# Performance work log

Hardware: AMD Instinct MI355X
Metric: run time of the kernel (lower is better)

## Reference

```python
import jax, jax.numpy as jnp
import numpy as np
import math

B, N, D = 128, 64, 2
H, M, L = 64, 64, 2
OMEGA = 1.0


def setup_inputs() -> dict:
    key = jax.random.key(0)
    ks = jax.random.split(key, 32)
    s = 0.1  # param scale
    rn = lambda k, shp: jax.random.normal(k, shp, dtype=jnp.float32) * s
    inp = {
        "x": jax.random.normal(ks[0], (B, N, D), dtype=jnp.float32),
        "spin": jnp.zeros((B, N, 1), jnp.float32),
        "node_w1": rn(ks[1], (D + 1, H)), "node_b1": rn(ks[2], (H,)),
        "node_w2": rn(ks[3], (H, H)), "node_b2": rn(ks[4], (H,)),
        "edge_w1": rn(ks[5], (D + 2, M)), "edge_b1": rn(ks[6], (M,)),
        "edge_w2": rn(ks[7], (M, M)), "edge_b2": rn(ks[8], (M,)),
        "v2e_w1": rn(ks[9], (L, H + M, M)), "v2e_b1": rn(ks[10], (L, M)),
        "v2e_w2": rn(ks[11], (L, M, M)), "v2e_b2": rn(ks[12], (L, M)),
        "e2v_w1": rn(ks[13], (L, M, H)), "e2v_b1": rn(ks[14], (L, H)),
        "e2v_w2": rn(ks[15], (L, H, H)), "e2v_b2": rn(ks[16], (L, H)),
        "head_w1": rn(ks[17], (H, H)), "head_b1": rn(ks[18], (H,)),
        "head_w2": rn(ks[19], (H, D)), "head_b2": rn(ks[20], (D,)),
        # bf_scale_init=0.3 -> softplus-inverse
        "scale": jnp.array([math.log(math.exp(0.3) - 1.0)], jnp.float32),
    }
    return inp


def _mlp(x, w1, b1, w2, b2, act):
    return act(x @ w1 + b1) @ w2 + b2


def reference(x, spin, node_w1, node_b1, node_w2, node_b2,
              edge_w1, edge_b1, edge_w2, edge_b2,
              v2e_w1, v2e_b1, v2e_w2, v2e_b2,
              e2v_w1, e2v_b1, e2v_w2, e2v_b2,
              head_w1, head_b1, head_w2, head_b2, scale):
    gelu = lambda t: jax.nn.gelu(t, approximate=False)  # torch exact GELU
    b, n, d = x.shape
    xs = x * jnp.float32(math.sqrt(OMEGA))
    # node embedding: [B,N,H]
    hv = _mlp(jnp.concatenate([xs, spin], -1), node_w1, node_b1, node_w2, node_b2, gelu)
    # dense pairwise edge features; dr[b,i,j] = xs[b,j] - xs[b,i]
    dr = xs[:, None, :, :] - xs[:, :, None, :]            # [B,N,N,D]
    r2 = jnp.sum(dr * dr, axis=-1, keepdims=True)          # [B,N,N,1]
    rr = jnp.sqrt(r2 + 1e-12)
    he = _mlp(jnp.concatenate([dr, rr, r2], -1), edge_w1, edge_b1, edge_w2, edge_b2, gelu)  # [B,N,N,M]
    # mask excludes self-edges (i==j) from aggregation (they were never created
    # in the original edge list; their dense entries never influence off-diag values)
    mask = (1.0 - jnp.eye(n, dtype=x.dtype))[None, :, :, None]
    inv = jnp.float32(1.0 / max(n - 1, 1))
    for l in range(v2e_w1.shape[0]):
        hvb = jnp.broadcast_to(hv[:, :, None, :], (b, n, n, hv.shape[-1]))  # source node i
        he = _mlp(jnp.concatenate([hvb, he], -1), v2e_w1[l], v2e_b1[l], v2e_w2[l], v2e_b2[l], gelu)
        m = _mlp(he, e2v_w1[l], e2v_b1[l], e2v_w2[l], e2v_b2[l], gelu)      # [B,N,N,H]
        hv = hv + jnp.sum(m * mask, axis=1) * inv           # scatter-add over sources i into j
    dx = _mlp(hv, head_w1, head_b1, head_w2, head_b2, jnp.tanh) * jax.nn.softplus(scale[0])
    return dx - jnp.mean(dx, axis=1, keepdims=True)
```

## Files before the change

kernel.cpp:

```cpp
#include <hip/hip_runtime.h>
#include <math.h>


typedef unsigned short u16;
typedef unsigned int u32;
typedef _Float16 half8 __attribute__((ext_vector_type(8)));
typedef __attribute__((ext_vector_type(4))) float floatx4;

#define TS 72
#define HROW 72
#define HBLK (64 * HROW)

__device__ __forceinline__ float gelu_f(float x) {
    float s = fabsf(x) * 0.70710678118654752f;
    float q = fmaf(fmaf(fmaf(fmaf(0.078108f, s, 0.000972f), s, 0.230389f), s, 0.278393f), s, 1.0f);
    float q2 = q * q;
    float r = __builtin_amdgcn_rcpf(q2 * q2);
    float t = 0.5f * x * r;
    return x > 0.f ? x - t : t;
}

__global__ __launch_bounds__(256) void k_pre(
    const float* __restrict__ ew2, const float* __restrict__ w1he0,
    const float* __restrict__ w2_0, const float* __restrict__ u1_0,
    const float* __restrict__ w1he1, const float* __restrict__ w2_1,
    const float* __restrict__ u1_1,
    const float* __restrict__ eb2, const float* __restrict__ b2_0,
    const float* __restrict__ c1_0, const float* __restrict__ b2_1,
    const float* __restrict__ c1_1,
    const float* __restrict__ b1_0v, const float* __restrict__ b1nv,
    const float* __restrict__ u2_0, const float* __restrict__ u2_1,
    const float* __restrict__ w1n, const float* __restrict__ hw1,
    _Float16* __restrict__ WF,
    float* __restrict__ biasB, float* __restrict__ biasC, float* __restrict__ biasD,
    float* __restrict__ u2_0T, float* __restrict__ u2_1T,
    float* __restrict__ w1nT, float* __restrict__ hw1T,
    const float* __restrict__ x, const float* __restrict__ spin,
    const float* __restrict__ nw1, const float* __restrict__ nb1,
    const float* __restrict__ nw2, const float* __restrict__ nb2,
    const float* __restrict__ w1_0,
    float* __restrict__ hv, float* __restrict__ p0)
{
    int blk = blockIdx.x;
    if (blk < 64) {
        int s = blk >> 4;
        int idx = (blk & 15) * 256 + threadIdx.x;
        int k = idx >> 6, n = idx & 63;
        const float *A, *Bm;
        if (s == 0)      { A = ew2;  Bm = w1he0; }
        else if (s == 1) { A = w2_0; Bm = u1_0;  }
        else if (s == 2) { A = w2_0; Bm = w1he1; }
        else             { A = w2_1; Bm = u1_1;  }
        float acc = 0.f;
        for (int q = 0; q < 64; ++q) acc = fmaf(A[k * 64 + q], Bm[q * 64 + n], acc);
        int kc = k >> 5, qd = (k >> 3) & 3, jj = k & 7;
        WF[(((s * 2 + kc) * 64 + n) * 4 + qd) * 8 + jj] = (_Float16)acc;
    } else if (blk == 64) {
        int s = threadIdx.x >> 6, cc = threadIdx.x & 63;
        if (s > 0) {
            const float *bv, *Bm, *add; float* dst;
            if (s == 1)      { bv = b2_0; Bm = u1_0;  add = c1_0; dst = biasB; }
            else if (s == 2) { bv = b2_0; Bm = w1he1; add = b1nv; dst = biasC; }
            else             { bv = b2_1; Bm = u1_1;  add = c1_1; dst = biasD; }
            float acc = add[cc];
            for (int q = 0; q < 64; ++q) acc = fmaf(bv[q], Bm[q * 64 + cc], acc);
            dst[cc] = acc;
        }
    } else if (blk < 129) {
        int idx = (blk - 65) * 256 + threadIdx.x;
        int s = idx >> 12, r = idx & 4095, m = r >> 6, tc = r & 63;
        const float* W = s == 0 ? u2_0 : s == 1 ? u2_1 : s == 2 ? w1n : hw1;
        float* WT      = s == 0 ? u2_0T : s == 1 ? u2_1T : s == 2 ? w1nT : hw1T;
        WT[tc * 64 + m] = W[m * 64 + tc];
    } else {
        __shared__ float a[4][64];
        __shared__ float shv[4][64];
        int w = threadIdx.x >> 6, h = threadIdx.x & 63;
        int node = (blk - 129) * 4 + w;
        float2 xv = ((const float2*)x)[node];
        float sp = spin[node];
        float z = fmaf(xv.x, nw1[h], fmaf(xv.y, nw1[64 + h], fmaf(sp, nw1[128 + h], nb1[h])));
        a[w][h] = gelu_f(z);
        float acc = nb2[h];
        for (int k = 0; k < 64; ++k) acc = fmaf(a[w][k], nw2[k * 64 + h], acc);
        hv[node * 64 + h] = acc;
        shv[w][h] = acc;
        float pa = b1_0v[h];
        for (int q = 0; q < 64; ++q) pa = fmaf(eb2[q], w1he0[q * 64 + h], pa);
        for (int k = 0; k < 64; ++k) pa = fmaf(shv[w][k], w1_0[k * 64 + h], pa);
        p0[node * 64 + h] = pa;
    }
}

__device__ __forceinline__ void mfma_acc(
    const _Float16* __restrict__ tA, const _Float16* __restrict__ WF,
    int stage, int c, int quad, int nn, floatx4 acc[4])
{
    int sA = ((nn >> 2) & 3) << 3;
    #pragma unroll
    for (int kc = 0; kc < 2; ++kc) {
        half8 bf = *(const half8*)(WF + (((stage * 2 + kc) * 64 + c) * 4 + quad) * 8);
        int k0 = (kc * 32 + quad * 8) ^ sA;
        #pragma unroll
        for (int mt = 0; mt < 4; ++mt) {
            half8 af = *(const half8*)(tA + (mt * 16 + nn) * TS + k0);
            acc[mt] = __builtin_amdgcn_mfma_f32_16x16x32_f16(af, bf, acc[mt], 0, 0, 0);
        }
    }
}

__device__ __forceinline__ void init_bias(floatx4 acc[4], float bc) {
    #pragma unroll
    for (int mt = 0; mt < 4; ++mt) acc[mt] = (floatx4){bc, bc, bc, bc};
}
__device__ __forceinline__ void init_p(floatx4 acc[4], const float* __restrict__ p,
                                       int rowbase, int c, int quad) {
    #pragma unroll
    for (int mt = 0; mt < 4; ++mt)
        #pragma unroll
        for (int r = 0; r < 4; ++r)
            acc[mt][r] = p[(rowbase + mt * 16 + quad * 4 + r) * 64 + c];
}

__global__ __launch_bounds__(256, 8) void k_L0(
    const float* __restrict__ x,
    const float* __restrict__ ew1, const float* __restrict__ eb1,
    const float* __restrict__ p0,
    const float* __restrict__ biasB,
    const float* __restrict__ u2_0T, const float* __restrict__ c2_0,
    const _Float16* __restrict__ WF,
    const float* __restrict__ hv0, float* __restrict__ hv1,
    const float* __restrict__ w1nT, const float* __restrict__ biasC,
    float* __restrict__ p1,
    u16* __restrict__ he0g)
{
    __shared__ __align__(16) _Float16 tA[64 * TS];
    __shared__ float sS[64];
    __shared__ float shv[64];
    __shared__ float sred[256];
    int t = threadIdx.x, L = t & 63;
    int w = __builtin_amdgcn_readfirstlane(t >> 6);
    int nn = L & 15, quad = L >> 4;
    int c = w * 16 + nn;
    int cw = c ^ (quad << 3);
    int b = blockIdx.x >> 6, j = blockIdx.x & 63;

    float2 xi = ((const float2*)x)[b * 64 + L];
    float2 xj = ((const float2*)x)[b * 64 + j];
    float d0 = xj.x - xi.x, d1 = xj.y - xi.y;
    float r2 = fmaf(d0, d0, d1 * d1);
    float rr = sqrtf(r2 + 1e-12f);
    int swL = ((L >> 2) & 3) << 3;

    #pragma unroll
    for (int mb = 0; mb < 2; ++mb) {
        int m0 = w * 16 + mb * 8;
        half8 h8;
        #pragma unroll
        for (int kk = 0; kk < 8; ++kk) {
            int m = m0 + kk;
            float z = fmaf(d0, ew1[m], fmaf(d1, ew1[64 + m],
                      fmaf(rr, ew1[128 + m], fmaf(r2, ew1[192 + m], eb1[m]))));
            h8[kk] = (_Float16)gelu_f(z);
        }
        *(half8*)(tA + L * TS + (m0 ^ swL)) = h8;
    }
    __syncthreads();

    floatx4 acc[4];
    init_p(acc, p0, b * 64, c, quad);
    mfma_acc(tA, WF, 0, c, quad, nn, acc);
    __syncthreads();
    {
        u16* dst = he0g + (size_t)blockIdx.x * HBLK;
        #pragma unroll
        for (int mt = 0; mt < 4; ++mt)
            #pragma unroll
            for (int r = 0; r < 4; ++r) {
                int i = mt * 16 + quad * 4 + r;
                _Float16 y = (_Float16)gelu_f(acc[mt][r]);
                tA[i * TS + cw] = y;
                dst[i * HROW + cw] = __builtin_bit_cast(u16, y);
            }
    }
    __syncthreads();
    init_bias(acc, biasB[c]);
    mfma_acc(tA, WF, 1, c, quad, nn, acc);
    {
        float s = 0.f;
        #pragma unroll
        for (int mt = 0; mt < 4; ++mt)
            #pragma unroll
            for (int r = 0; r < 4; ++r) {
                int i = mt * 16 + quad * 4 + r;
                float g = gelu_f(acc[mt][r]);
                s += (i == j) ? 0.f : g;
            }
        s += __shfl_xor(s, 16);
        s += __shfl_xor(s, 32);
        if (quad == 0) sS[c] = s;
    }
    __syncthreads();
    {
        const float4* sv4 = (const float4*)(sS + w * 16);
        const float4* uv4 = (const float4*)(u2_0T + L * 64 + w * 16);
        float g = 0.f;
        #pragma unroll
        for (int m4 = 0; m4 < 4; ++m4) {
            float4 sv = sv4[m4], uv = uv4[m4];
            g = fmaf(sv.x, uv.x, fmaf(sv.y, uv.y, fmaf(sv.z, uv.z, fmaf(sv.w, uv.w, g))));
        }
        sred[w * 64 + L] = g;
    }
    __syncthreads();
    if (t < 64) {
        float g = sred[t] + sred[64 + t] + sred[128 + t] + sred[192 + t];
        int o = blockIdx.x * 64 + t;
        float hvv = hv0[o] + g * (1.0f / 63.0f) + c2_0[t];
        hv1[o] = hvv;
        shv[t] = hvv;
    }
    __syncthreads();
    {
        const float4* hv4 = (const float4*)(shv + w * 16);
        const float4* wv4 = (const float4*)(w1nT + L * 64 + w * 16);
        float pa = 0.f;
        #pragma unroll
        for (int m4 = 0; m4 < 4; ++m4) {
            float4 sv = hv4[m4], uv = wv4[m4];
            pa = fmaf(sv.x, uv.x, fmaf(sv.y, uv.y, fmaf(sv.z, uv.z, fmaf(sv.w, uv.w, pa))));
        }
        sred[w * 64 + L] = pa;
    }
    __syncthreads();
    if (t < 64)
        p1[blockIdx.x * 64 + t] = biasC[t] + sred[t] + sred[64 + t] + sred[128 + t] + sred[192 + t];
}

__global__ __launch_bounds__(256, 8) void k_L1(
    const u16* __restrict__ he0g,
    const float* __restrict__ p1,
    const float* __restrict__ biasD,
    const float* __restrict__ u2_1T, const float* __restrict__ c2_1,
    const _Float16* __restrict__ WF,
    const float* __restrict__ hv1,
    const float* __restrict__ hw1T, const float* __restrict__ hb1,
    const float* __restrict__ hw2, const float* __restrict__ hb2,
    const float* __restrict__ scale, float* __restrict__ dx)
{
    __shared__ __align__(16) _Float16 tA[64 * TS];
    __shared__ float sS[64];
    __shared__ float shv[64];
    __shared__ float sred[256];
    int t = threadIdx.x, L = t & 63;
    int w = __builtin_amdgcn_readfirstlane(t >> 6);
    int nn = L & 15, quad = L >> 4;
    int c = w * 16 + nn;
    int cw = c ^ (quad << 3);
    int b = blockIdx.x >> 6, j = blockIdx.x & 63;

    {
        const float4* src = (const float4*)(he0g + (size_t)blockIdx.x * HBLK);
        float4* dstl = (float4*)tA;
        for (int q = t; q < (HBLK * 2 / 16); q += 256)
            dstl[q] = src[q];
    }
    __syncthreads();

    floatx4 acc[4];
    init_p(acc, p1, b * 64, c, quad);
    mfma_acc(tA, WF, 2, c, quad, nn, acc);
    __syncthreads();
    #pragma unroll
    for (int mt = 0; mt < 4; ++mt)
        #pragma unroll
        for (int r = 0; r < 4; ++r)
            tA[(mt * 16 + quad * 4 + r) * TS + cw] = (_Float16)gelu_f(acc[mt][r]);
    __syncthreads();
    init_bias(acc, biasD[c]);
    mfma_acc(tA, WF, 3, c, quad, nn, acc);
    {
        float s = 0.f;
        #pragma unroll
        for (int mt = 0; mt < 4; ++mt)
            #pragma unroll
            for (int r = 0; r < 4; ++r) {
                int i = mt * 16 + quad * 4 + r;
                float g = gelu_f(acc[mt][r]);
                s += (i == j) ? 0.f : g;
            }
        s += __shfl_xor(s, 16);
        s += __shfl_xor(s, 32);
        if (quad == 0) sS[c] = s;
    }
    __syncthreads();
    {
        const float4* sv4 = (const float4*)(sS + w * 16);
        const float4* uv4 = (const float4*)(u2_1T + L * 64 + w * 16);
        float g = 0.f;
        #pragma unroll
        for (int m4 = 0; m4 < 4; ++m4) {
            float4 sv = sv4[m4], uv = uv4[m4];
            g = fmaf(sv.x, uv.x, fmaf(sv.y, uv.y, fmaf(sv.z, uv.z, fmaf(sv.w, uv.w, g))));
        }
        sred[w * 64 + L] = g;
    }
    __syncthreads();
    if (t < 64) {
        float g = sred[t] + sred[64 + t] + sred[128 + t] + sred[192 + t];
        float hv2 = hv1[blockIdx.x * 64 + t] + g * (1.0f / 63.0f) + c2_1[t];
        shv[t] = hv2;
    }
    __syncthreads();
    {
        const float4* hv4 = (const float4*)(shv + w * 16);
        const float4* wv4 = (const float4*)(hw1T + L * 64 + w * 16);
        float a = 0.f;
        #pragma unroll
        for (int m4 = 0; m4 < 4; ++m4) {
            float4 sv = hv4[m4], uv = wv4[m4];
            a = fmaf(sv.x, uv.x, fmaf(sv.y, uv.y, fmaf(sv.z, uv.z, fmaf(sv.w, uv.w, a))));
        }
        sred[w * 64 + L] = a;
    }
    __syncthreads();
    if (t < 64) {
        float a = hb1[t] + sred[t] + sred[64 + t] + sred[128 + t] + sred[192 + t];
        float t1 = tanhf(a);
        float dd0 = t1 * hw2[t * 2], dd1 = t1 * hw2[t * 2 + 1];
        #pragma unroll
        for (int off = 1; off <= 32; off <<= 1) { dd0 += __shfl_xor(dd0, off); dd1 += __shfl_xor(dd1, off); }
        if (t == 0) {
            float sp = log1pf(__expf(scale[0]));
            dx[blockIdx.x * 2 + 0] = (dd0 + hb2[0]) * sp;
            dx[blockIdx.x * 2 + 1] = (dd1 + hb2[1]) * sp;
        }
    }
}

__global__ __launch_bounds__(64) void k_mean(
    const float* __restrict__ dx, float* __restrict__ out)
{
    __shared__ float s0[64], s1[64];
    int b = blockIdx.x, j = threadIdx.x;
    float2 d = ((const float2*)dx)[b * 64 + j];
    s0[j] = d.x; s1[j] = d.y;
    __syncthreads();
    float m0 = 0.f, m1 = 0.f;
    for (int q = 0; q < 64; ++q) { m0 += s0[q]; m1 += s1[q]; }
    ((float2*)out)[b * 64 + j] = make_float2(d.x - m0 * (1.0f / 64.0f), d.y - m1 * (1.0f / 64.0f));
}

__global__ void k_beacon(float* out, float code) { out[0] = code; }

extern "C" void kernel_launch(void* const* d_in, const int* in_sizes, int n_in,
                              void* d_out, int out_size, void* d_ws, size_t ws_size,
                              hipStream_t stream)
{
    static const int exp_sizes[23] = {
        16384, 8192, 192, 64, 4096, 64,
        256, 64, 4096, 64,
        16384, 128, 8192, 128,
        8192, 128, 8192, 128,
        4096, 64, 128, 2, 1
    };
    float* hv0 = (float*)d_ws;
    float* hv1 = hv0 + 524288;
    float* p0  = hv1 + 524288;
    float* p1  = p0  + 524288;
    float* dx  = p1  + 524288;
    float* u2_0T = dx + 16384;
    float* u2_1T = u2_0T + 4096;
    float* w1nT  = u2_1T + 4096;
    float* hw1T  = w1nT + 4096;
    float* biasB = hw1T + 4096;
    float* biasC = biasB + 64;
    float* biasD = biasC + 64;
    _Float16* WF = (_Float16*)(biasD + 64);
    u16* he0g  = (u16*)(WF + 16384);
    const size_t need = (size_t)((char*)(he0g + (size_t)8192 * HBLK) - (char*)d_ws);

    int bad = -1;
    if (n_in != 23 || out_size != 16384) bad = 98;
    else if (ws_size < need) bad = 97;
    else for (int i = 0; i < 23; ++i)
        if (in_sizes[i] != exp_sizes[i]) { bad = i; break; }
    if (bad >= 0) {
        k_beacon<<<1, 1, 0, stream>>>((float*)d_out, 2e6f + bad * 1e4f);
        return;
    }

    const float* x      = (const float*)d_in[0];
    const float* spin   = (const float*)d_in[1];
    const float* nw1    = (const float*)d_in[2];
    const float* nb1    = (const float*)d_in[3];
    const float* nw2    = (const float*)d_in[4];
    const float* nb2    = (const float*)d_in[5];
    const float* ew1    = (const float*)d_in[6];
    const float* eb1    = (const float*)d_in[7];
    const float* ew2    = (const float*)d_in[8];
    const float* eb2    = (const float*)d_in[9];
    const float* v2e_w1 = (const float*)d_in[10];
    const float* v2e_b1 = (const float*)d_in[11];
    const float* v2e_w2 = (const float*)d_in[12];
    const float* v2e_b2 = (const float*)d_in[13];
    const float* e2v_w1 = (const float*)d_in[14];
    const float* e2v_b1 = (const float*)d_in[15];
    const float* e2v_w2 = (const float*)d_in[16];
    const float* e2v_b2 = (const float*)d_in[17];
    const float* hw1    = (const float*)d_in[18];
    const float* hb1    = (const float*)d_in[19];
    const float* hw2    = (const float*)d_in[20];
    const float* hb2    = (const float*)d_in[21];
    const float* scale  = (const float*)d_in[22];

    k_pre<<<2177, 256, 0, stream>>>(
        ew2, v2e_w1 + 4096, v2e_w2, e2v_w1,
        v2e_w1 + 12288, v2e_w2 + 4096, e2v_w1 + 4096,
        eb2, v2e_b2, e2v_b1, v2e_b2 + 64, e2v_b1 + 64,
        v2e_b1, v2e_b1 + 64,
        e2v_w2, e2v_w2 + 4096, v2e_w1 + 8192, hw1,
        WF, biasB, biasC, biasD,
        u2_0T, u2_1T, w1nT, hw1T,
        x, spin, nw1, nb1, nw2, nb2, v2e_w1, hv0, p0);
    k_L0<<<8192, 256, 0, stream>>>(x, ew1, eb1,
        p0, biasB, u2_0T, e2v_b2,
        WF, hv0, hv1,
        w1nT, biasC, p1,
        he0g);
    k_L1<<<8192, 256, 0, stream>>>(he0g,
        p1, biasD, u2_1T, e2v_b2 + 64,
        WF, hv1, hw1T, hb1, hw2, hb2, scale, dx);
    k_mean<<<128, 64, 0, stream>>>(dx, (float*)d_out);
}
```

Before: 224.4 us.

## Transpose p buffers, vectorize GELU pairs, and bulk-copy he0 tile to global

```diff
diff --git a/kernel.cpp b/kernel.cpp
--- a/kernel.cpp
+++ b/kernel.cpp
@@ -6,10 +6,10 @@
 typedef unsigned int u32;
 typedef _Float16 half8 __attribute__((ext_vector_type(8)));
 typedef __attribute__((ext_vector_type(4))) float floatx4;
+typedef float f32x2 __attribute__((ext_vector_type(2)));
 
 #define TS 72
-#define HROW 72
-#define HBLK (64 * HROW)
+#define HBLK (64 * TS)
 
 __device__ __forceinline__ float gelu_f(float x) {
     float s = fabsf(x) * 0.70710678118654752f;
@@ -18,6 +18,17 @@
     float r = __builtin_amdgcn_rcpf(q2 * q2);
     float t = 0.5f * x * r;
     return x > 0.f ? x - t : t;
+}
+
+__device__ __forceinline__ f32x2 gelu2p(f32x2 x) {
+    f32x2 ax; ax.x = fabsf(x.x); ax.y = fabsf(x.y);
+    f32x2 s = ax * 0.70710678118654752f;
+    f32x2 q = (((s * 0.078108f + 0.000972f) * s + 0.230389f) * s + 0.278393f) * s + 1.0f;
+    f32x2 q2 = q * q;
+    f32x2 q4 = q2 * q2;
+    f32x2 r; r.x = __builtin_amdgcn_rcpf(q4.x); r.y = __builtin_amdgcn_rcpf(q4.y);
+    f32x2 t = x + ax - ax * r;
+    return t * 0.5f;
 }
 
 __global__ __launch_bounds__(256) void k_pre(
@@ -39,7 +50,7 @@
     const float* __restrict__ nw1, const float* __restrict__ nb1,
     const float* __restrict__ nw2, const float* __restrict__ nb2,
     const float* __restrict__ w1_0,
-    float* __restrict__ hv, float* __restrict__ p0)
+    float* __restrict__ hv, float* __restrict__ p0T)
 {
     int blk = blockIdx.x;
     if (blk < 64) {
@@ -88,7 +99,7 @@
         float pa = b1_0v[h];
         for (int q = 0; q < 64; ++q) pa = fmaf(eb2[q], w1he0[q * 64 + h], pa);
         for (int k = 0; k < 64; ++k) pa = fmaf(shv[w][k], w1_0[k * 64 + h], pa);
-        p0[node * 64 + h] = pa;
+        p0T[((node & ~63) + h) * 64 + (node & 63)] = pa;
     }
 }
 
@@ -113,25 +124,25 @@
     #pragma unroll
     for (int mt = 0; mt < 4; ++mt) acc[mt] = (floatx4){bc, bc, bc, bc};
 }
-__device__ __forceinline__ void init_p(floatx4 acc[4], const float* __restrict__ p,
-                                       int rowbase, int c, int quad) {
-    #pragma unroll
-    for (int mt = 0; mt < 4; ++mt)
-        #pragma unroll
-        for (int r = 0; r < 4; ++r)
-            acc[mt][r] = p[(rowbase + mt * 16 + quad * 4 + r) * 64 + c];
+__device__ __forceinline__ void init_pT(floatx4 acc[4], const float* __restrict__ pT,
+                                        int b64c, int quad) {
+    #pragma unroll
+    for (int mt = 0; mt < 4; ++mt) {
+        float4 v = *(const float4*)(pT + b64c * 64 + mt * 16 + quad * 4);
+        acc[mt] = (floatx4){v.x, v.y, v.z, v.w};
+    }
 }
 
 __global__ __launch_bounds__(256, 8) void k_L0(
     const float* __restrict__ x,
     const float* __restrict__ ew1, const float* __restrict__ eb1,
-    const float* __restrict__ p0,
+    const float* __restrict__ p0T,
     const float* __restrict__ biasB,
     const float* __restrict__ u2_0T, const float* __restrict__ c2_0,
     const _Float16* __restrict__ WF,
     const float* __restrict__ hv0, float* __restrict__ hv1,
     const float* __restrict__ w1nT, const float* __restrict__ biasC,
-    float* __restrict__ p1,
+    float* __restrict__ p1T,
     u16* __restrict__ he0g)
 {
     __shared__ __align__(16) _Float16 tA[64 * TS];
@@ -157,50 +168,60 @@
         int m0 = w * 16 + mb * 8;
         half8 h8;
         #pragma unroll
-        for (int kk = 0; kk < 8; ++kk) {
+        for (int kk = 0; kk < 8; kk += 2) {
             int m = m0 + kk;
-            float z = fmaf(d0, ew1[m], fmaf(d1, ew1[64 + m],
-                      fmaf(rr, ew1[128 + m], fmaf(r2, ew1[192 + m], eb1[m]))));
-            h8[kk] = (_Float16)gelu_f(z);
+            f32x2 z;
+            z.x = fmaf(d0, ew1[m], fmaf(d1, ew1[64 + m],
+                  fmaf(rr, ew1[128 + m], fmaf(r2, ew1[192 + m], eb1[m]))));
+            z.y = fmaf(d0, ew1[m + 1], fmaf(d1, ew1[64 + m + 1],
+                  fmaf(rr, ew1[128 + m + 1], fmaf(r2, ew1[192 + m + 1], eb1[m + 1]))));
+            f32x2 g = gelu2p(z);
+            h8[kk] = (_Float16)g.x;
+            h8[kk + 1] = (_Float16)g.y;
         }
         *(half8*)(tA + L * TS + (m0 ^ swL)) = h8;
     }
     __syncthreads();
 
     floatx4 acc[4];
-    init_p(acc, p0, b * 64, c, quad);
+    init_pT(acc, p0T, b * 64 + c, quad);
     mfma_acc(tA, WF, 0, c, quad, nn, acc);
     __syncthreads();
-    {
-        u16* dst = he0g + (size_t)blockIdx.x * HBLK;
+    #pragma unroll
+    for (int mt = 0; mt < 4; ++mt)
+        #pragma unroll
+        for (int rp = 0; rp < 4; rp += 2) {
+            f32x2 v; v.x = acc[mt][rp]; v.y = acc[mt][rp + 1];
+            f32x2 g = gelu2p(v);
+            int i = mt * 16 + quad * 4 + rp;
+            tA[i * TS + cw]       = (_Float16)g.x;
+            tA[(i + 1) * TS + cw] = (_Float16)g.y;
+        }
+    __syncthreads();
+    init_bias(acc, biasB[c]);
+    mfma_acc(tA, WF, 1, c, quad, nn, acc);
+    {
+        float s = 0.f;
         #pragma unroll
         for (int mt = 0; mt < 4; ++mt)
             #pragma unroll
-            for (int r = 0; r < 4; ++r) {
-                int i = mt * 16 + quad * 4 + r;
-                _Float16 y = (_Float16)gelu_f(acc[mt][r]);
-                tA[i * TS + cw] = y;
-                dst[i * HROW + cw] = __builtin_bit_cast(u16, y);
-            }
-    }
-    __syncthreads();
-    init_bias(acc, biasB[c]);
-    mfma_acc(tA, WF, 1, c, quad, nn, acc);
-    {
-        float s = 0.f;
-        #pragma unroll
-        for (int mt = 0; mt < 4; ++mt)
-            #pragma unroll
-            for (int r = 0; r < 4; ++r) {
-                int i = mt * 16 + quad * 4 + r;
-                float g = gelu_f(acc[mt][r]);
-                s += (i == j) ? 0.f : g;
+            for (int rp = 0; rp < 4; rp += 2) {
+                int i = mt * 16 + quad * 4 + rp;
+                f32x2 v; v.x = acc[mt][rp]; v.y = acc[mt][rp + 1];
+                f32x2 g = gelu2p(v);
+                s += (i == j ? 0.f : g.x) + (i + 1 == j ? 0.f : g.y);
             }
         s += __shfl_xor(s, 16);
         s += __shfl_xor(s, 32);
         if (quad == 0) sS[c] = s;
     }
     __syncthreads();
+    {
+        const float4* src = (const float4*)tA;
+        float4* dst = (float4*)(he0g + (size_t)blockIdx.x * HBLK);
+        for (int q = t; q < (HBLK * 2 / 16); q += 256)
+            dst[q] = src[q];
+    }
     {
         const float4* sv4 = (const float4*)(sS + w * 16);
         const float4* uv4 = (const float4*)(u2_0T + L * 64 + w * 16);
@@ -234,12 +255,13 @@
     }
     __syncthreads();
     if (t < 64)
-        p1[blockIdx.x * 64 + t] = biasC[t] + sred[t] + sred[64 + t] + sred[128 + t] + sred[192 + t];
+        p1T[((blockIdx.x & ~63) + t) * 64 + (blockIdx.x & 63)] =
+            biasC[t] + sred[t] + sred[64 + t] + sred[128 + t] + sred[192 + t];
 }
 
 __global__ __launch_bounds__(256, 8) void k_L1(
     const u16* __restrict__ he0g,
-    const float* __restrict__ p1,
+    const float* __restrict__ p1T,
     const float* __restrict__ biasD,
     const float* __restrict__ u2_1T, const float* __restrict__ c2_1,
     const _Float16* __restrict__ WF,
@@ -268,14 +290,19 @@
     __syncthreads();
 
     floatx4 acc[4];
-    init_p(acc, p1, b * 64, c, quad);
+    init_pT(acc, p1T, b * 64 + c, quad);
     mfma_acc(tA, WF, 2, c, quad, nn, acc);
     __syncthreads();
     #pragma unroll
     for (int mt = 0; mt < 4; ++mt)
         #pragma unroll
-        for (int r = 0; r < 4; ++r)
-            tA[(mt * 16 + quad * 4 + r) * TS + cw] = (_Float16)gelu_f(acc[mt][r]);
+        for (int rp = 0; rp < 4; rp += 2) {
+            f32x2 v; v.x = acc[mt][rp]; v.y = acc[mt][rp + 1];
+            f32x2 g = gelu2p(v);
+            int i = mt * 16 + quad * 4 + rp;
+            tA[i * TS + cw]       = (_Float16)g.x;
+            tA[(i + 1) * TS + cw] = (_Float16)g.y;
+        }
     __syncthreads();
     init_bias(acc, biasD[c]);
     mfma_acc(tA, WF, 3, c, quad, nn, acc);
@@ -284,10 +311,11 @@
         #pragma unroll
         for (int mt = 0; mt < 4; ++mt)
             #pragma unroll
-            for (int r = 0; r < 4; ++r) {
-                int i = mt * 16 + quad * 4 + r;
-                float g = gelu_f(acc[mt][r]);
-                s += (i == j) ? 0.f : g;
+            for (int rp = 0; rp < 4; rp += 2) {
+                int i = mt * 16 + quad * 4 + rp;
+                f32x2 v; v.x = acc[mt][rp]; v.y = acc[mt][rp + 1];
+                f32x2 g = gelu2p(v);
+                s += (i == j ? 0.f : g.x) + (i + 1 == j ? 0.f : g.y);
             }
         s += __shfl_xor(s, 16);
         s += __shfl_xor(s, 32);
@@ -366,9 +394,9 @@
     };
     float* hv0 = (float*)d_ws;
     float* hv1 = hv0 + 524288;
-    float* p0  = hv1 + 524288;
-    float* p1  = p0  + 524288;
-    float* dx  = p1  + 524288;
+    float* p0T = hv1 + 524288;
+    float* p1T = p0T + 524288;
+    float* dx  = p1T + 524288;
     float* u2_0T = dx + 16384;
     float* u2_1T = u2_0T + 4096;
     float* w1nT  = u2_1T + 4096;
@@ -422,14 +450,14 @@
         e2v_w2, e2v_w2 + 4096, v2e_w1 + 8192, hw1,
         WF, biasB, biasC, biasD,
         u2_0T, u2_1T, w1nT, hw1T,
-        x, spin, nw1, nb1, nw2, nb2, v2e_w1, hv0, p0);
+        x, spin, nw1, nb1, nw2, nb2, v2e_w1, hv0, p0T);
     k_L0<<<8192, 256, 0, stream>>>(x, ew1, eb1,
-        p0, biasB, u2_0T, e2v_b2,
+        p0T, biasB, u2_0T, e2v_b2,
         WF, hv0, hv1,
-        w1nT, biasC, p1,
+        w1nT, biasC, p1T,
         he0g);
     k_L1<<<8192, 256, 0, stream>>>(he0g,
-        p1, biasD, u2_1T, e2v_b2 + 64,
+        p1T, biasD, u2_1T, e2v_b2 + 64,
         WF, hv1, hw1T, hb1, hw2, hb2, scale, dx);
     k_mean<<<128, 64, 0, stream>>>(dx, (float*)d_out);
 }
```

Result: slower. 238.8 us (+6.4%).
